# Kernel tuning notes

Measured on AMD Instinct MI355X. Metric: run time of the kernel, lower is better.

The kernel has to match this reference:

```python
import jax, jax.numpy as jnp
import numpy as np

silu = jax.nn.silu
B, L, H, IN = 128, 2048, 8, 37
NL = 8  # 4 encoder + 4 decoder SE3 layers, stacked


def _se3_layer(h, pos, eW1, eb1, eW2, eb2, pW1, pb1, pW2, nW1, nb1, nW2, nb2):
    # chain graph: row = 0..N-2, col = 1..N-1 (as in the torch arange edges)
    rel = pos[1:] - pos[:-1]                      # [N-1, 3]
    dist = jnp.linalg.norm(rel, axis=-1, keepdims=True)
    ef = jnp.concatenate([h[:-1], h[1:], dist], axis=-1)   # [N-1, 2H+1]
    ea = silu(ef @ eW1 + eb1) @ eW2 + eb2                   # edge_mlp
    dp = silu(ea @ pW1 + pb1) @ pW2                         # pos_mlp (no bias on last)
    pos_upd = jnp.zeros_like(pos).at[:-1].add(dp).at[1:].add(-dp)
    node_upd = jnp.zeros_like(h).at[:-1].add(ea).at[1:].add(ea)
    h_out = silu(jnp.concatenate([h, node_upd], axis=-1) @ nW1 + nb1) @ nW2 + nb2
    return h_out, pos + 0.1 * pos_upd


def setup_inputs() -> dict:
    key = jax.random.key(0)
    ks = jax.random.split(key, 64)
    i = iter(range(64))
    def p(shape, s=0.1):
        return (jax.random.normal(ks[next(i)], shape, jnp.float32) * s)
    inp = {
        "atom_positions": jax.random.normal(ks[next(i)], (B, L, IN, 3), jnp.float32),
        "atom_mask": (jax.random.uniform(ks[next(i)], (B, L, IN)) < 0.8).astype(jnp.float32),
        "emb_W": p((IN, H)), "emb_b": p((H,)),
        "posemb_W1": p((3, H)), "posemb_b1": p((H,)),
        "posemb_W2": p((H, H)), "posemb_b2": p((H,)),
        # stacked SE3 conv params: layers 0-3 encoder, 4-7 decoder
        "conv_eW1": p((NL, 2 * H + 1, H)), "conv_eb1": p((NL, H)),
        "conv_eW2": p((NL, H, H)), "conv_eb2": p((NL, H)),
        "conv_pW1": p((NL, H, H)), "conv_pb1": p((NL, H)),
        "conv_pW2": p((NL, H, 3)),
        "conv_nW1": p((NL, 2 * H, H)), "conv_nb1": p((NL, H)),
        "conv_nW2": p((NL, H, H)), "conv_nb2": p((NL, H)),
        "tol_W1": p((H, H)), "tol_b1": p((H,)),
        "tol_W2": p((H, H)), "tol_b2": p((H,)),
        "froml_W1": p((H, H)), "froml_b1": p((H,)),
        "froml_W2": p((H, H)), "froml_b2": p((H,)),
        "posdec_W1": p((H, 2 * H)), "posdec_b1": p((2 * H,)),
        "posdec_W2": p((2 * H, IN * 3)), "posdec_b2": p((IN * 3,)),
        "maskdec_W": p((H, IN)), "maskdec_b": p((IN,)),
    }
    return inp


def reference(atom_positions, atom_mask, emb_W, emb_b, posemb_W1, posemb_b1,
              posemb_W2, posemb_b2, conv_eW1, conv_eb1, conv_eW2, conv_eb2,
              conv_pW1, conv_pb1, conv_pW2, conv_nW1, conv_nb1, conv_nW2,
              conv_nb2, tol_W1, tol_b1, tol_W2, tol_b2, froml_W1, froml_b1,
              froml_W2, froml_b2, posdec_W1, posdec_b1, posdec_W2, posdec_b2,
              maskdec_W, maskdec_b):
    # ---- encode ----
    h = atom_mask @ emb_W + emb_b                              # [B,L,H]
    m = atom_mask[..., None]
    mean_pos = (atom_positions * m).sum(axis=2) / (m.sum(axis=2) + 1e-8)  # [B,L,3]
    pos_feat = silu(mean_pos @ posemb_W1 + posemb_b1) @ posemb_W2 + posemb_b2
    h = (h + pos_feat).reshape(B * L, H)
    pos = mean_pos.reshape(B * L, 3)
    for li in range(4):
        h, pos = _se3_layer(h, pos, conv_eW1[li], conv_eb1[li], conv_eW2[li],
                            conv_eb2[li], conv_pW1[li], conv_pb1[li], conv_pW2[li],
                            conv_nW1[li], conv_nb1[li], conv_nW2[li], conv_nb2[li])
    h = h.reshape(B, L, H)
    z = silu(h @ tol_W1 + tol_b1) @ tol_W2 + tol_b2            # [B,L,latent]
    # ---- decode ----
    h = silu(z @ froml_W1 + froml_b1) @ froml_W2 + froml_b2
    h = h.reshape(B * L, H)
    pos = pos  # already flat [B*L, 3]
    for li in range(4, 8):
        h, pos = _se3_layer(h, pos, conv_eW1[li], conv_eb1[li], conv_eW2[li],
                            conv_eb2[li], conv_pW1[li], conv_pb1[li], conv_pW2[li],
                            conv_nW1[li], conv_nb1[li], conv_nW2[li], conv_nb2[li])
    h = h.reshape(B, L, H)
    pos_out = (silu(h @ posdec_W1 + posdec_b1) @ posdec_W2 + posdec_b2)
    pos_out = pos_out.reshape(B, L, IN, 3)
    mask_out = h @ maskdec_W + maskdec_b                       # [B,L,IN]
    return pos_out, mask_out
```

## Files before the change

### kernel.cpp

```cpp
#include <hip/hip_runtime.h>

#define NTOT 262144
#define NLAY 8
#define TOUT 240

__device__ __forceinline__ float silu_f(float x) {
    return x * (1.0f / (1.0f + __expf(-x)));
}

__global__ __launch_bounds__(256) void k_encode(
    const float* __restrict__ ap, const float* __restrict__ amask,
    const float* __restrict__ embW, const float* __restrict__ embB,
    const float* __restrict__ peW1, const float* __restrict__ peB1,
    const float* __restrict__ peW2, const float* __restrict__ peB2,
    float* __restrict__ h0, float* __restrict__ pos0)
{
    __shared__ alignas(16) float sM[64 * 37];
    __shared__ alignas(16) float sA[64 * 111];
    __shared__ alignas(16) float sW[37 * 8];
    const int tid = threadIdx.x;
    const long nb = (long)blockIdx.x * 64;

    if (tid < 74) ((float4*)sW)[tid] = ((const float4*)embW)[tid];
    const float4* gm = (const float4*)(amask + nb * 37);
    float4* sm4 = (float4*)sM;
    #pragma unroll 1
    for (int i = tid; i < 64 * 37 / 4; i += 256) sm4[i] = gm[i];
    const float4* ga = (const float4*)(ap + nb * 111);
    float4* sa4 = (float4*)sA;
    #pragma unroll 1
    for (int i = tid; i < 64 * 111 / 4; i += 256) sa4[i] = ga[i];
    __syncthreads();

    const int n = tid >> 2;
    const int p = tid & 3;
    const int k0 = p * 10;
    const int k1 = (p == 3) ? 37 : k0 + 10;

    const float* mrow = sM + n * 37;
    const float* arow = sA + n * 111;
    float hacc[8] = {0, 0, 0, 0, 0, 0, 0, 0};
    float ps0 = 0.f, ps1 = 0.f, ps2 = 0.f, msum = 0.f;
    #pragma unroll 1
    for (int k = k0; k < k1; ++k) {
        float mv = mrow[k];
        msum += mv;
        const float4* wr = (const float4*)(sW + k * 8);
        float4 w0 = wr[0], w1 = wr[1];
        hacc[0] += mv * w0.x; hacc[1] += mv * w0.y;
        hacc[2] += mv * w0.z; hacc[3] += mv * w0.w;
        hacc[4] += mv * w1.x; hacc[5] += mv * w1.y;
        hacc[6] += mv * w1.z; hacc[7] += mv * w1.w;
        ps0 += mv * arow[k * 3 + 0];
        ps1 += mv * arow[k * 3 + 1];
        ps2 += mv * arow[k * 3 + 2];
    }
    #pragma unroll
    for (int m = 1; m <= 2; m <<= 1) {
        msum += __shfl_xor(msum, m);
        ps0 += __shfl_xor(ps0, m);
        ps1 += __shfl_xor(ps1, m);
        ps2 += __shfl_xor(ps2, m);
        #pragma unroll
        for (int j = 0; j < 8; ++j) hacc[j] += __shfl_xor(hacc[j], m);
    }

    float inv = 1.0f / (msum + 1e-8f);
    float mp0 = ps0 * inv, mp1 = ps1 * inv, mp2 = ps2 * inv;
    float q[8];
    #pragma unroll
    for (int j = 0; j < 8; ++j) {
        float a = peB1[j];
        a += mp0 * peW1[0 * 8 + j];
        a += mp1 * peW1[1 * 8 + j];
        a += mp2 * peW1[2 * 8 + j];
        q[j] = silu_f(a);
    }
    #pragma unroll
    for (int j = 0; j < 8; ++j) {
        float a = peB2[j] + embB[j];
        #pragma unroll
        for (int r = 0; r < 8; ++r) a += q[r] * peW2[r * 8 + j];
        hacc[j] += a;
    }
    const long g = nb + n;
    if (p == 0) ((float4*)(h0 + g * 8))[0] = make_float4(hacc[0], hacc[1], hacc[2], hacc[3]);
    if (p == 1) ((float4*)(h0 + g * 8))[1] = make_float4(hacc[4], hacc[5], hacc[6], hacc[7]);
    if (p == 2) ((float4*)pos0)[g] = make_float4(mp0, mp1, mp2, 0.f);
}

__global__ __launch_bounds__(256) void k_stack(
    const float* __restrict__ h0, const float* __restrict__ pos0,
    float* __restrict__ hfin,
    const float* __restrict__ ceW1, const float* __restrict__ ceB1,
    const float* __restrict__ ceW2, const float* __restrict__ ceB2,
    const float* __restrict__ cpW1, const float* __restrict__ cpB1,
    const float* __restrict__ cpW2,
    const float* __restrict__ cnW1, const float* __restrict__ cnB1,
    const float* __restrict__ cnW2, const float* __restrict__ cnB2,
    const float* __restrict__ tW1, const float* __restrict__ tB1,
    const float* __restrict__ tW2, const float* __restrict__ tB2,
    const float* __restrict__ fW1, const float* __restrict__ fB1,
    const float* __restrict__ fW2, const float* __restrict__ fB2)
{
    __shared__ float4 sH[512];
    __shared__ float4 sP[256];
    __shared__ float4 sE[512];
    __shared__ float4 sD[256];
    const int t = threadIdx.x;
    const int g0 = blockIdx.x * TOUT;
    const int g = g0 - 8 + t;

    float4 z4 = make_float4(0.f, 0.f, 0.f, 0.f);
    float4 ha = z4, hb = z4, pa = z4;
    if (g >= 0 && g < NTOT) {
        const float4* hp = (const float4*)(h0 + (long)g * 8);
        ha = hp[0];
        hb = hp[1];
        pa = ((const float4*)pos0)[g];
    }
    sH[t * 2] = ha;
    sH[t * 2 + 1] = hb;
    sP[t] = pa;
    __syncthreads();

    const int tp = (t < 255) ? (t + 1) : t;
    const int tm = (t > 0) ? (t - 1) : t;
    float hn[8] = {0, 0, 0, 0, 0, 0, 0, 0};

    #pragma unroll 1
    for (int li = 0; li < NLAY; ++li) {
        float hl[8], hr[8];
        {
            float4 a = sH[t * 2], b = sH[t * 2 + 1];
            hl[0] = a.x; hl[1] = a.y; hl[2] = a.z; hl[3] = a.w;
            hl[4] = b.x; hl[5] = b.y; hl[6] = b.z; hl[7] = b.w;
            float4 c = sH[tp * 2], d = sH[tp * 2 + 1];
            hr[0] = c.x; hr[1] = c.y; hr[2] = c.z; hr[3] = c.w;
            hr[4] = d.x; hr[5] = d.y; hr[6] = d.z; hr[7] = d.w;
        }
        float4 plv = sP[t], prv = sP[tp];
        float r0 = prv.x - plv.x, r1 = prv.y - plv.y, r2 = prv.z - plv.z;
        float dist = sqrtf(r0 * r0 + r1 * r1 + r2 * r2);

        const float* wE1 = ceW1 + li * 136;
        const float* bE1 = ceB1 + li * 8;
        const float* wE2 = ceW2 + li * 64;
        const float* bE2 = ceB2 + li * 8;
        const float* wP1 = cpW1 + li * 64;
        const float* bP1 = cpB1 + li * 8;
        const float* wP2 = cpW2 + li * 24;
        const float* wN1 = cnW1 + li * 128;
        const float* bN1 = cnB1 + li * 8;
        const float* wN2 = cnW2 + li * 64;
        const float* bN2 = cnB2 + li * 8;

        float t1[8];
        #pragma unroll
        for (int j = 0; j < 8; ++j) {
            float a = bE1[j];
            #pragma unroll
            for (int r = 0; r < 8; ++r) a += hl[r] * wE1[r * 8 + j];
            #pragma unroll
            for (int r = 0; r < 8; ++r) a += hr[r] * wE1[64 + r * 8 + j];
            a += dist * wE1[128 + j];
            t1[j] = silu_f(a);
        }
        float ea[8];
        #pragma unroll
        for (int j = 0; j < 8; ++j) {
            float a = bE2[j];
            #pragma unroll
            for (int r = 0; r < 8; ++r) a += t1[r] * wE2[r * 8 + j];
            ea[j] = a;
        }
        float q[8];
        #pragma unroll
        for (int j = 0; j < 8; ++j) {
            float a = bP1[j];
            #pragma unroll
            for (int r = 0; r < 8; ++r) a += ea[r] * wP1[r * 8 + j];
            q[j] = silu_f(a);
        }
        float dp0 = 0.f, dp1 = 0.f, dp2 = 0.f;
        #pragma unroll
        for (int r = 0; r < 8; ++r) {
            dp0 += q[r] * wP2[r * 3 + 0];
            dp1 += q[r] * wP2[r * 3 + 1];
            dp2 += q[r] * wP2[r * 3 + 2];
        }
        sE[t * 2] = make_float4(ea[0], ea[1], ea[2], ea[3]);
        sE[t * 2 + 1] = make_float4(ea[4], ea[5], ea[6], ea[7]);
        sD[t] = make_float4(dp0, dp1, dp2, 0.f);
        __syncthreads();

        float nu[8] = {0, 0, 0, 0, 0, 0, 0, 0};
        float pu0 = 0.f, pu1 = 0.f, pu2 = 0.f;
        if (g < NTOT - 1) {
            #pragma unroll
            for (int j = 0; j < 8; ++j) nu[j] += ea[j];
            pu0 += dp0; pu1 += dp1; pu2 += dp2;
        }
        if (g > 0) {
            float4 a = sE[tm * 2], b = sE[tm * 2 + 1];
            nu[0] += a.x; nu[1] += a.y; nu[2] += a.z; nu[3] += a.w;
            nu[4] += b.x; nu[5] += b.y; nu[6] += b.z; nu[7] += b.w;
            float4 dl = sD[tm];
            pu0 -= dl.x; pu1 -= dl.y; pu2 -= dl.z;
        }
        float u[8];
        #pragma unroll
        for (int j = 0; j < 8; ++j) {
            float a = bN1[j];
            #pragma unroll
            for (int r = 0; r < 8; ++r) a += hl[r] * wN1[r * 8 + j];
            #pragma unroll
            for (int r = 0; r < 8; ++r) a += nu[r] * wN1[64 + r * 8 + j];
            u[j] = silu_f(a);
        }
        #pragma unroll
        for (int j = 0; j < 8; ++j) {
            float a = bN2[j];
            #pragma unroll
            for (int r = 0; r < 8; ++r) a += u[r] * wN2[r * 8 + j];
            hn[j] = a;
        }
        float pn0 = plv.x + 0.1f * pu0;
        float pn1 = plv.y + 0.1f * pu1;
        float pn2 = plv.z + 0.1f * pu2;

        if (li == 3) {
            float a8[8];
            #pragma unroll
            for (int j = 0; j < 8; ++j) {
                float a = tB1[j];
                #pragma unroll
                for (int r = 0; r < 8; ++r) a += hn[r] * tW1[r * 8 + j];
                a8[j] = silu_f(a);
            }
            float zz[8];
            #pragma unroll
            for (int j = 0; j < 8; ++j) {
                float a = tB2[j];
                #pragma unroll
                for (int r = 0; r < 8; ++r) a += a8[r] * tW2[r * 8 + j];
                zz[j] = a;
            }
            float b8[8];
            #pragma unroll
            for (int j = 0; j < 8; ++j) {
                float a = fB1[j];
                #pragma unroll
                for (int r = 0; r < 8; ++r) a += zz[r] * fW1[r * 8 + j];
                b8[j] = silu_f(a);
            }
            #pragma unroll
            for (int j = 0; j < 8; ++j) {
                float a = fB2[j];
                #pragma unroll
                for (int r = 0; r < 8; ++r) a += b8[r] * fW2[r * 8 + j];
                hn[j] = a;
            }
        }

        const int winLo2 = max(0, g0 - 7 + li);
        const int winHi2 = min(NTOT, g0 + 247 - li);
        if (g >= winLo2 && g < winHi2) {
            sH[t * 2] = make_float4(hn[0], hn[1], hn[2], hn[3]);
            sH[t * 2 + 1] = make_float4(hn[4], hn[5], hn[6], hn[7]);
            sP[t] = make_float4(pn0, pn1, pn2, 0.f);
        }
        __syncthreads();
    }

    if (t >= 8 && t < 8 + TOUT && g < NTOT) {
        float4* hd = (float4*)(hfin + (long)g * 8);
        hd[0] = make_float4(hn[0], hn[1], hn[2], hn[3]);
        hd[1] = make_float4(hn[4], hn[5], hn[6], hn[7]);
    }
}

__global__ __launch_bounds__(256) void k_decode(
    const float* __restrict__ hfin,
    const float* __restrict__ dW1, const float* __restrict__ dB1,
    const float* __restrict__ dW2, const float* __restrict__ dB2,
    const float* __restrict__ mW, const float* __restrict__ mB,
    float* __restrict__ out)
{
    __shared__ alignas(16) float sh[128 * 8];
    __shared__ alignas(16) float st1[128 * 16];
    const int tid = threadIdx.x;
    const long nb = (long)blockIdx.x * 128;

    ((float4*)sh)[tid] = ((const float4*)(hfin + nb * 8))[tid];
    __syncthreads();

    {
        const int n = tid >> 1;
        const int c0 = (tid & 1) * 8;
        const float4* h4 = (const float4*)(sh + n * 8);
        float4 h0v = h4[0], h1v = h4[1];
        float hr[8] = {h0v.x, h0v.y, h0v.z, h0v.w, h1v.x, h1v.y, h1v.z, h1v.w};
        #pragma unroll
        for (int jj = 0; jj < 8; ++jj) {
            int j = c0 + jj;
            float a = dB1[j];
            #pragma unroll
            for (int r = 0; r < 8; ++r) a += hr[r] * dW1[r * 16 + j];
            st1[n * 16 + j] = silu_f(a);
        }
    }
    __syncthreads();

    if (tid < 222) {
        const int half = (tid >= 111) ? 1 : 0;
        const int j = tid - half * 111;
        float w[16];
        #pragma unroll
        for (int r = 0; r < 16; ++r) w[r] = dW2[r * 111 + j];
        const float bj = dB2[j];
        float* op = out + nb * 111 + j;
        #pragma unroll 2
        for (int n = half; n < 128; n += 2) {
            const float4* t4 = (const float4*)(st1 + n * 16);
            float4 a0 = t4[0], a1 = t4[1], a2 = t4[2], a3 = t4[3];
            float acc = bj;
            acc += a0.x * w[0] + a0.y * w[1] + a0.z * w[2] + a0.w * w[3];
            acc += a1.x * w[4] + a1.y * w[5] + a1.z * w[6] + a1.w * w[7];
            acc += a2.x * w[8] + a2.y * w[9] + a2.z * w[10] + a2.w * w[11];
            acc += a3.x * w[12] + a3.y * w[13] + a3.z * w[14] + a3.w * w[15];
            op[n * 111] = acc;
        }
        const int g6 = tid / 37;
        const int j2 = tid - g6 * 37;
        float wm[8];
        #pragma unroll
        for (int r = 0; r < 8; ++r) wm[r] = mW[r * 37 + j2];
        const float bm = mB[j2];
        float* omp_ = out + (long)NTOT * 111 + nb * 37 + j2;
        #pragma unroll 1
        for (int n = g6; n < 128; n += 6) {
            const float4* h4 = (const float4*)(sh + n * 8);
            float4 h0v = h4[0], h1v = h4[1];
            float acc = bm;
            acc += h0v.x * wm[0] + h0v.y * wm[1] + h0v.z * wm[2] + h0v.w * wm[3];
            acc += h1v.x * wm[4] + h1v.y * wm[5] + h1v.z * wm[6] + h1v.w * wm[7];
            omp_[n * 37] = acc;
        }
    }
}

extern "C" void kernel_launch(void* const* d_in, const int* in_sizes, int n_in,
                              void* d_out, int out_size, void* d_ws, size_t ws_size,
                              hipStream_t stream) {
    const float* ap     = (const float*)d_in[0];
    const float* amask  = (const float*)d_in[1];
    const float* embW   = (const float*)d_in[2];
    const float* embB   = (const float*)d_in[3];
    const float* peW1   = (const float*)d_in[4];
    const float* peB1   = (const float*)d_in[5];
    const float* peW2   = (const float*)d_in[6];
    const float* peB2   = (const float*)d_in[7];
    const float* ceW1   = (const float*)d_in[8];
    const float* ceB1   = (const float*)d_in[9];
    const float* ceW2   = (const float*)d_in[10];
    const float* ceB2   = (const float*)d_in[11];
    const float* cpW1   = (const float*)d_in[12];
    const float* cpB1   = (const float*)d_in[13];
    const float* cpW2   = (const float*)d_in[14];
    const float* cnW1   = (const float*)d_in[15];
    const float* cnB1   = (const float*)d_in[16];
    const float* cnW2   = (const float*)d_in[17];
    const float* cnB2   = (const float*)d_in[18];
    const float* tW1    = (const float*)d_in[19];
    const float* tB1    = (const float*)d_in[20];
    const float* tW2    = (const float*)d_in[21];
    const float* tB2    = (const float*)d_in[22];
    const float* fW1    = (const float*)d_in[23];
    const float* fB1    = (const float*)d_in[24];
    const float* fW2    = (const float*)d_in[25];
    const float* fB2    = (const float*)d_in[26];
    const float* dW1    = (const float*)d_in[27];
    const float* dB1    = (const float*)d_in[28];
    const float* dW2    = (const float*)d_in[29];
    const float* dB2    = (const float*)d_in[30];
    const float* mW     = (const float*)d_in[31];
    const float* mB     = (const float*)d_in[32];

    float* h0   = (float*)d_ws;
    float* pos0 = h0 + (size_t)NTOT * 8;
    float* hfin = pos0 + (size_t)NTOT * 4;
    float* out  = (float*)d_out;

    k_encode<<<NTOT / 64, 256, 0, stream>>>(ap, amask, embW, embB,
                                            peW1, peB1, peW2, peB2, h0, pos0);
    k_stack<<<(NTOT + TOUT - 1) / TOUT, 256, 0, stream>>>(
        h0, pos0, hfin,
        ceW1, ceB1, ceW2, ceB2, cpW1, cpB1, cpW2,
        cnW1, cnB1, cnW2, cnB2,
        tW1, tB1, tW2, tB2, fW1, fB1, fW2, fB2);
    k_decode<<<NTOT / 128, 256, 0, stream>>>(hfin, dW1, dB1, dW2, dB2, mW, mB, out);
}
```

Baseline: 433.7 us.

## Fuse encode, SE3 stack and decode into a single kernel

Merges the three kernels into one. Encoding is computed per node inside the stack block's halo window, and decoding reads directly from the shared h buffer, so the h0/pos0/hfin global round trips and two launches go away. The cost is that halo nodes (16 per 240) are encoded redundantly. The encode step now has one thread loop over all 37 atoms with uncoalesced per-thread global reads instead of cooperative staging in shared memory. Shared memory is reused across phases through a union buffer.

Result: slower. 668.7 us (+54.2%).

```diff
diff --git a/kernel.cpp b/kernel.cpp
--- a/kernel.cpp
+++ b/kernel.cpp
@@ -8,90 +8,11 @@
     return x * (1.0f / (1.0f + __expf(-x)));
 }
 
-__global__ __launch_bounds__(256) void k_encode(
+__global__ __launch_bounds__(256) void k_fused(
     const float* __restrict__ ap, const float* __restrict__ amask,
     const float* __restrict__ embW, const float* __restrict__ embB,
     const float* __restrict__ peW1, const float* __restrict__ peB1,
     const float* __restrict__ peW2, const float* __restrict__ peB2,
-    float* __restrict__ h0, float* __restrict__ pos0)
-{
-    __shared__ alignas(16) float sM[64 * 37];
-    __shared__ alignas(16) float sA[64 * 111];
-    __shared__ alignas(16) float sW[37 * 8];
-    const int tid = threadIdx.x;
-    const long nb = (long)blockIdx.x * 64;
-
-    if (tid < 74) ((float4*)sW)[tid] = ((const float4*)embW)[tid];
-    const float4* gm = (const float4*)(amask + nb * 37);
-    float4* sm4 = (float4*)sM;
-    #pragma unroll 1
-    for (int i = tid; i < 64 * 37 / 4; i += 256) sm4[i] = gm[i];
-    const float4* ga = (const float4*)(ap + nb * 111);
-    float4* sa4 = (float4*)sA;
-    #pragma unroll 1
-    for (int i = tid; i < 64 * 111 / 4; i += 256) sa4[i] = ga[i];
-    __syncthreads();
-
-    const int n = tid >> 2;
-    const int p = tid & 3;
-    const int k0 = p * 10;
-    const int k1 = (p == 3) ? 37 : k0 + 10;
-
-    const float* mrow = sM + n * 37;
-    const float* arow = sA + n * 111;
-    float hacc[8] = {0, 0, 0, 0, 0, 0, 0, 0};
-    float ps0 = 0.f, ps1 = 0.f, ps2 = 0.f, msum = 0.f;
-    #pragma unroll 1
-    for (int k = k0; k < k1; ++k) {
-        float mv = mrow[k];
-        msum += mv;
-        const float4* wr = (const float4*)(sW + k * 8);
-        float4 w0 = wr[0], w1 = wr[1];
-        hacc[0] += mv * w0.x; hacc[1] += mv * w0.y;
-        hacc[2] += mv * w0.z; hacc[3] += mv * w0.w;
-        hacc[4] += mv * w1.x; hacc[5] += mv * w1.y;
-        hacc[6] += mv * w1.z; hacc[7] += mv * w1.w;
-        ps0 += mv * arow[k * 3 + 0];
-        ps1 += mv * arow[k * 3 + 1];
-        ps2 += mv * arow[k * 3 + 2];
-    }
-    #pragma unroll
-    for (int m = 1; m <= 2; m <<= 1) {
-        msum += __shfl_xor(msum, m);
-        ps0 += __shfl_xor(ps0, m);
-        ps1 += __shfl_xor(ps1, m);
-        ps2 += __shfl_xor(ps2, m);
-        #pragma unroll
-        for (int j = 0; j < 8; ++j) hacc[j] += __shfl_xor(hacc[j], m);
-    }
-
-    float inv = 1.0f / (msum + 1e-8f);
-    float mp0 = ps0 * inv, mp1 = ps1 * inv, mp2 = ps2 * inv;
-    float q[8];
-    #pragma unroll
-    for (int j = 0; j < 8; ++j) {
-        float a = peB1[j];
-        a += mp0 * peW1[0 * 8 + j];
-        a += mp1 * peW1[1 * 8 + j];
-        a += mp2 * peW1[2 * 8 + j];
-        q[j] = silu_f(a);
-    }
-    #pragma unroll
-    for (int j = 0; j < 8; ++j) {
-        float a = peB2[j] + embB[j];
-        #pragma unroll
-        for (int r = 0; r < 8; ++r) a += q[r] * peW2[r * 8 + j];
-        hacc[j] += a;
-    }
-    const long g = nb + n;
-    if (p == 0) ((float4*)(h0 + g * 8))[0] = make_float4(hacc[0], hacc[1], hacc[2], hacc[3]);
-    if (p == 1) ((float4*)(h0 + g * 8))[1] = make_float4(hacc[4], hacc[5], hacc[6], hacc[7]);
-    if (p == 2) ((float4*)pos0)[g] = make_float4(mp0, mp1, mp2, 0.f);
-}
-
-__global__ __launch_bounds__(256) void k_stack(
-    const float* __restrict__ h0, const float* __restrict__ pos0,
-    float* __restrict__ hfin,
     const float* __restrict__ ceW1, const float* __restrict__ ceB1,
     const float* __restrict__ ceW2, const float* __restrict__ ceB2,
     const float* __restrict__ cpW1, const float* __restrict__ cpB1,
@@ -101,27 +22,77 @@
     const float* __restrict__ tW1, const float* __restrict__ tB1,
     const float* __restrict__ tW2, const float* __restrict__ tB2,
     const float* __restrict__ fW1, const float* __restrict__ fB1,
-    const float* __restrict__ fW2, const float* __restrict__ fB2)
+    const float* __restrict__ fW2, const float* __restrict__ fB2,
+    const float* __restrict__ dW1, const float* __restrict__ dB1,
+    const float* __restrict__ dW2, const float* __restrict__ dB2,
+    const float* __restrict__ mW, const float* __restrict__ mB,
+    float* __restrict__ out)
 {
     __shared__ float4 sH[512];
     __shared__ float4 sP[256];
-    __shared__ float4 sE[512];
-    __shared__ float4 sD[256];
+    __shared__ alignas(16) char SC[15360];
+    float4* sE = (float4*)SC;
+    float4* sD = (float4*)(SC + 8192);
+    float*  st1 = (float*)SC;
+    float*  sW  = (float*)SC;
+
     const int t = threadIdx.x;
     const int g0 = blockIdx.x * TOUT;
     const int g = g0 - 8 + t;
-
-    float4 z4 = make_float4(0.f, 0.f, 0.f, 0.f);
-    float4 ha = z4, hb = z4, pa = z4;
-    if (g >= 0 && g < NTOT) {
-        const float4* hp = (const float4*)(h0 + (long)g * 8);
-        ha = hp[0];
-        hb = hp[1];
-        pa = ((const float4*)pos0)[g];
-    }
-    sH[t * 2] = ha;
-    sH[t * 2 + 1] = hb;
-    sP[t] = pa;
+    const bool vg = (g >= 0 && g < NTOT);
+
+    if (t < 74) ((float4*)sW)[t] = ((const float4*)embW)[t];
+    __syncthreads();
+
+    float hacc[8] = {0, 0, 0, 0, 0, 0, 0, 0};
+    float ps0 = 0.f, ps1 = 0.f, ps2 = 0.f, msum = 0.f;
+    if (vg) {
+        const float* mrow = amask + (long)g * 37;
+        const float* arow = ap + (long)g * 111;
+        #pragma unroll 2
+        for (int k = 0; k < 37; ++k) {
+            float mv = mrow[k];
+            msum += mv;
+            const float4* wr = (const float4*)(sW + k * 8);
+            float4 w0 = wr[0], w1 = wr[1];
+            hacc[0] += mv * w0.x; hacc[1] += mv * w0.y;
+            hacc[2] += mv * w0.z; hacc[3] += mv * w0.w;
+            hacc[4] += mv * w1.x; hacc[5] += mv * w1.y;
+            hacc[6] += mv * w1.z; hacc[7] += mv * w1.w;
+            ps0 += mv * arow[k * 3 + 0];
+            ps1 += mv * arow[k * 3 + 1];
+            ps2 += mv * arow[k * 3 + 2];
+        }
+    }
+    float inv = 1.0f / (msum + 1e-8f);
+    float mp0 = ps0 * inv, mp1 = ps1 * inv, mp2 = ps2 * inv;
+    {
+        float q[8];
+        #pragma unroll
+        for (int j = 0; j < 8; ++j) {
+            float a = peB1[j];
+            a += mp0 * peW1[0 * 8 + j];
+            a += mp1 * peW1[1 * 8 + j];
+            a += mp2 * peW1[2 * 8 + j];
+            q[j] = silu_f(a);
+        }
+        #pragma unroll
+        for (int j = 0; j < 8; ++j) {
+            float a = peB2[j] + embB[j];
+            #pragma unroll
+            for (int r = 0; r < 8; ++r) a += q[r] * peW2[r * 8 + j];
+            hacc[j] += a;
+        }
+    }
+    __syncthreads();
+    if (vg) {
+        sH[t * 2]     = make_float4(hacc[0], hacc[1], hacc[2], hacc[3]);
+        sH[t * 2 + 1] = make_float4(hacc[4], hacc[5], hacc[6], hacc[7]);
+        sP[t] = make_float4(mp0, mp1, mp2, 0.f);
+    } else {
+        float4 z = make_float4(0.f, 0.f, 0.f, 0.f);
+        sH[t * 2] = z; sH[t * 2 + 1] = z; sP[t] = z;
+    }
     __syncthreads();
 
     const int tp = (t < 255) ? (t + 1) : t;
@@ -273,55 +244,37 @@
         __syncthreads();
     }
 
-    if (t >= 8 && t < 8 + TOUT && g < NTOT) {
-        float4* hd = (float4*)(hfin + (long)g * 8);
-        hd[0] = make_float4(hn[0], hn[1], hn[2], hn[3]);
-        hd[1] = make_float4(hn[4], hn[5], hn[6], hn[7]);
-    }
-}
-
-__global__ __launch_bounds__(256) void k_decode(
-    const float* __restrict__ hfin,
-    const float* __restrict__ dW1, const float* __restrict__ dB1,
-    const float* __restrict__ dW2, const float* __restrict__ dB2,
-    const float* __restrict__ mW, const float* __restrict__ mB,
-    float* __restrict__ out)
-{
-    __shared__ alignas(16) float sh[128 * 8];
-    __shared__ alignas(16) float st1[128 * 16];
-    const int tid = threadIdx.x;
-    const long nb = (long)blockIdx.x * 128;
-
-    ((float4*)sh)[tid] = ((const float4*)(hfin + nb * 8))[tid];
+    #pragma unroll 1
+    for (int idx = t; idx < 480; idx += 256) {
+        const int w = idx >> 1;
+        const int c0 = (idx & 1) * 8;
+        if (g0 + w < NTOT) {
+            const float4* h4 = (const float4*)&sH[(w + 8) * 2];
+            float4 h0v = h4[0], h1v = h4[1];
+            float hr[8] = {h0v.x, h0v.y, h0v.z, h0v.w, h1v.x, h1v.y, h1v.z, h1v.w};
+            #pragma unroll
+            for (int jj = 0; jj < 8; ++jj) {
+                int j = c0 + jj;
+                float a = dB1[j];
+                #pragma unroll
+                for (int r = 0; r < 8; ++r) a += hr[r] * dW1[r * 16 + j];
+                st1[w * 16 + j] = silu_f(a);
+            }
+        }
+    }
     __syncthreads();
 
-    {
-        const int n = tid >> 1;
-        const int c0 = (tid & 1) * 8;
-        const float4* h4 = (const float4*)(sh + n * 8);
-        float4 h0v = h4[0], h1v = h4[1];
-        float hr[8] = {h0v.x, h0v.y, h0v.z, h0v.w, h1v.x, h1v.y, h1v.z, h1v.w};
-        #pragma unroll
-        for (int jj = 0; jj < 8; ++jj) {
-            int j = c0 + jj;
-            float a = dB1[j];
-            #pragma unroll
-            for (int r = 0; r < 8; ++r) a += hr[r] * dW1[r * 16 + j];
-            st1[n * 16 + j] = silu_f(a);
-        }
-    }
-    __syncthreads();
-
-    if (tid < 222) {
-        const int half = (tid >= 111) ? 1 : 0;
-        const int j = tid - half * 111;
+    if (t < 222) {
+        const int half = (t >= 111) ? 1 : 0;
+        const int j = t - half * 111;
         float w[16];
         #pragma unroll
         for (int r = 0; r < 16; ++r) w[r] = dW2[r * 111 + j];
         const float bj = dB2[j];
-        float* op = out + nb * 111 + j;
+        float* op = out + (long)g0 * 111 + j;
         #pragma unroll 2
-        for (int n = half; n < 128; n += 2) {
+        for (int n = half; n < TOUT; n += 2) {
+            if (g0 + n >= NTOT) break;
             const float4* t4 = (const float4*)(st1 + n * 16);
             float4 a0 = t4[0], a1 = t4[1], a2 = t4[2], a3 = t4[3];
             float acc = bj;
@@ -331,16 +284,17 @@
             acc += a3.x * w[12] + a3.y * w[13] + a3.z * w[14] + a3.w * w[15];
             op[n * 111] = acc;
         }
-        const int g6 = tid / 37;
-        const int j2 = tid - g6 * 37;
+        const int g6 = t / 37;
+        const int j2 = t - g6 * 37;
         float wm[8];
         #pragma unroll
         for (int r = 0; r < 8; ++r) wm[r] = mW[r * 37 + j2];
         const float bm = mB[j2];
-        float* omp_ = out + (long)NTOT * 111 + nb * 37 + j2;
+        float* omp_ = out + (long)NTOT * 111 + (long)g0 * 37 + j2;
         #pragma unroll 1
-        for (int n = g6; n < 128; n += 6) {
-            const float4* h4 = (const float4*)(sh + n * 8);
+        for (int n = g6; n < TOUT; n += 6) {
+            if (g0 + n >= NTOT) break;
+            const float4* h4 = (const float4*)&sH[(n + 8) * 2];
             float4 h0v = h4[0], h1v = h4[1];
             float acc = bm;
             acc += h0v.x * wm[0] + h0v.y * wm[1] + h0v.z * wm[2] + h0v.w * wm[3];
@@ -386,18 +340,13 @@
     const float* dB2    = (const float*)d_in[30];
     const float* mW     = (const float*)d_in[31];
     const float* mB     = (const float*)d_in[32];
-
-    float* h0   = (float*)d_ws;
-    float* pos0 = h0 + (size_t)NTOT * 8;
-    float* hfin = pos0 + (size_t)NTOT * 4;
-    float* out  = (float*)d_out;
-
-    k_encode<<<NTOT / 64, 256, 0, stream>>>(ap, amask, embW, embB,
-                                            peW1, peB1, peW2, peB2, h0, pos0);
-    k_stack<<<(NTOT + TOUT - 1) / TOUT, 256, 0, stream>>>(
-        h0, pos0, hfin,
+    float* out = (float*)d_out;
+
+    const int nblk = (NTOT + TOUT - 1) / TOUT;
+    k_fused<<<nblk, 256, 0, stream>>>(
+        ap, amask, embW, embB, peW1, peB1, peW2, peB2,
         ceW1, ceB1, ceW2, ceB2, cpW1, cpB1, cpW2,
         cnW1, cnB1, cnW2, cnB2,
-        tW1, tB1, tW2, tB2, fW1, fB1, fW2, fB2);
-    k_decode<<<NTOT / 128, 256, 0, stream>>>(hfin, dW1, dB1, dW2, dB2, mW, mB, out);
+        tW1, tB1, tW2, tB2, fW1, fB1, fW2, fB2,
+        dW1, dB1, dW2, dB2, mW, mB, out);
 }
```
